# Optimization experiments

Hardware: AMD Instinct MI355X
Metric: run time of the kernel (lower is better)

The kernel has to match this reference:

```python
import jax, jax.numpy as jnp
import numpy as np

NUM_TAGS = 9
INNER_DIM = 64
HIDDEN = 768
MASK_VAL = 1e12


def setup_inputs() -> dict:
    key = jax.random.key(0)
    k1, k2, k3, k4 = jax.random.split(key, 4)
    B, S = 16, 512
    encoder_output = jax.random.normal(k1, (B, S, HIDDEN), dtype=jnp.float32)
    token_ids = jax.random.randint(k2, (B, S), 0, 30000, dtype=jnp.int64)
    attention_mask = jnp.ones((B, S), dtype=jnp.int32)
    W = jax.random.normal(k3, (HIDDEN, NUM_TAGS * INNER_DIM * 2), dtype=jnp.float32) * 0.02
    b = jax.random.normal(k4, (NUM_TAGS * INNER_DIM * 2,), dtype=jnp.float32) * 0.02
    return {"encoder_output": encoder_output, "token_ids": token_ids,
            "attention_mask": attention_mask, "W": W, "b": b}


def _rope_sin_cos(seq_len, dim, dtype):
    # sinusoidal position embedding, interleaved then repeat_interleave(2)
    pos = jnp.arange(seq_len, dtype=dtype)[:, None]              # [S,1]
    inv = jnp.power(10000.0, -2.0 * jnp.arange(dim // 2, dtype=dtype) / dim)
    ang = pos * inv                                              # [S,d/2]
    sin = jnp.repeat(jnp.sin(ang), 2, axis=-1)                   # [S,d]
    cos = jnp.repeat(jnp.cos(ang), 2, axis=-1)                   # [S,d]
    return sin, cos


def _rotate_half(x):
    # stack([-x[...,1::2], x[...,::2]], -1).reshape(x.shape)
    x2 = jnp.stack([-x[..., 1::2], x[..., ::2]], axis=-1)
    return x2.reshape(x.shape)


def reference(encoder_output, token_ids, attention_mask, W, b):
    B, S, _ = encoder_output.shape
    d = INNER_DIM
    out = encoder_output @ W + b                                 # [B,S,T*2d]
    out = out.reshape(B, S, NUM_TAGS, 2 * d)
    qw, kw = out[..., :d], out[..., d:]                          # [B,S,T,d]

    sin, cos = _rope_sin_cos(S, d, encoder_output.dtype)
    sin = sin[None, :, None, :]                                  # [1,S,1,d]
    cos = cos[None, :, None, :]
    qw = qw * cos + _rotate_half(qw) * sin
    kw = kw * cos + _rotate_half(kw) * sin

    logits = jnp.einsum('bshd,bthd->bhst', qw, kw)               # [B,T,S,S]

    pad = attention_mask.astype(logits.dtype)[:, None, None, :]  # key-side mask
    logits = logits * pad - (1.0 - pad) * MASK_VAL
    tril = jnp.tril(jnp.ones((S, S), dtype=logits.dtype), -1)
    logits = logits - tril * MASK_VAL
    return logits / jnp.sqrt(jnp.asarray(d, logits.dtype))
```

## Files before the change

kernel.cpp:

```cpp
#include <hip/hip_runtime.h>

#define MASK_VALF 1000000000000.0f

typedef __attribute__((ext_vector_type(8))) short s16x8;
typedef __attribute__((ext_vector_type(4))) float f32x4;

__device__ __forceinline__ unsigned f2bf_u(float f) {
    union { float f; unsigned u; } v; v.f = f;
    return (v.u + 0x7FFFu + ((v.u >> 16) & 1u)) >> 16;
}
__device__ __forceinline__ short f2bf(float f) { return (short)(f2bf_u(f) & 0xFFFFu); }

#define GLOAD16(gp, lp) __builtin_amdgcn_global_load_lds( \
    (const __attribute__((address_space(1))) void*)(gp),  \
    (__attribute__((address_space(3))) void*)(lp), 16, 0, 0)

__global__ __launch_bounds__(256) void prep_all(
    const float* __restrict__ enc, short* __restrict__ encb,
    const float* __restrict__ W, short* __restrict__ wtb,
    float* __restrict__ scf)
{
    const int blk = blockIdx.x;
    const int t = threadIdx.x;
    if (blk < 6144) {
        int i = blk * 256 + t;
        float4 v = ((const float4*)enc)[i];
        short4 o;
        o.x = f2bf(v.x); o.y = f2bf(v.y); o.z = f2bf(v.z); o.w = f2bf(v.w);
        ((short4*)encb)[i] = o;
    } else if (blk < 7008) {
        __shared__ float tile[32][33];
        int tb = blk - 6144;
        int tbx = tb % 36;
        int tby = tb / 36;
        int tx = t & 31, ty = t >> 5;
#pragma unroll
        for (int r = 0; r < 4; ++r) {
            int row = ty + r * 8;
            tile[row][tx] = W[(tby * 32 + row) * 1152 + tbx * 32 + tx];
        }
        __syncthreads();
#pragma unroll
        for (int r = 0; r < 4; ++r) {
            int row = ty + r * 8;
            wtb[(size_t)(tbx * 32 + row) * 768 + tby * 32 + tx] = f2bf(tile[tx][row]);
        }
    } else {
        int id = (blk - 7008) * 256 + t;
        int pos = id >> 5, j = id & 31;
        float inv = powf(10000.0f, -2.0f * (float)j / 64.0f);
        float ang = (float)pos * inv;
        float s, c;
        sincosf(ang, &s, &c);
        scf[id * 2]     = c;
        scf[id * 2 + 1] = s;
    }
}

__global__ __launch_bounds__(256) void gemm1_rope(
    const short* __restrict__ A,
    const short* __restrict__ Bt,
    const float* __restrict__ bias,
    const float* __restrict__ scf,
    short* __restrict__ qk)
{
    __shared__ __align__(16) short As[128 * 32];
    __shared__ __align__(16) short Bs[128 * 32];
    const int t = threadIdx.x;
    const int w = t >> 6, lane = t & 63;
    const int lr = lane & 15, quad = lane >> 4;
    const int wm = w >> 1, wn = w & 1;
    const int m0 = blockIdx.y * 128;
    const int n0 = blockIdx.x * 128;

    f32x4 acc[4][4] = {};

    const short* gA = A  + (size_t)(m0 + (t >> 2)) * 768 + (t & 3) * 8;
    const short* gB = Bt + (size_t)(n0 + (t >> 2)) * 768 + (t & 3) * 8;
    short* lA0 = &As[w * 512];
    short* lA1 = &As[2048 + w * 512];
    short* lB0 = &Bs[w * 512];
    short* lB1 = &Bs[2048 + w * 512];

    for (int kt = 0; kt < 24; ++kt) {
        __syncthreads();
        GLOAD16(gA,            lA0);
        GLOAD16(gA + 64 * 768, lA1);
        GLOAD16(gB,            lB0);
        GLOAD16(gB + 64 * 768, lB1);
        gA += 32; gB += 32;
        __syncthreads();

        s16x8 af[4], bw[4];
#pragma unroll
        for (int i = 0; i < 4; ++i)
            af[i] = *(const s16x8*)&Bs[(wm * 64 + i * 16 + lr) * 32 + quad * 8];
#pragma unroll
        for (int j = 0; j < 4; ++j)
            bw[j] = *(const s16x8*)&As[(wn * 64 + j * 16 + lr) * 32 + quad * 8];
#pragma unroll
        for (int i = 0; i < 4; ++i)
#pragma unroll
            for (int j = 0; j < 4; ++j)
                acc[i][j] = __builtin_amdgcn_mfma_f32_16x16x32_bf16(af[i], bw[j], acc[i][j], 0, 0, 0);
    }

#pragma unroll
    for (int i = 0; i < 4; ++i) {
        const int colg0 = n0 + wm * 64 + i * 16 + quad * 4;
        const float4 bv = *(const float4*)&bias[colg0];
        const int tag = colg0 >> 7;
        const int qkf = (colg0 >> 6) & 1;
        const int dd0 = colg0 & 63;
        const int jj0 = dd0 >> 1;
        short* qbase = qk + ((size_t)tag * 2 + qkf) * 512 * 64 + dd0;
#pragma unroll
        for (int j = 0; j < 4; ++j) {
            const int rowg = m0 + wn * 64 + j * 16 + lr;
            const int bidx = rowg >> 9;
            const int pos  = rowg & 511;
            const float4 cs = *(const float4*)&scf[pos * 64 + jj0 * 2];
            float x0 = acc[i][j][0] + bv.x;
            float x1 = acc[i][j][1] + bv.y;
            float x2 = acc[i][j][2] + bv.z;
            float x3 = acc[i][j][3] + bv.w;
            float o0 = x0 * cs.x - x1 * cs.y;
            float o1 = x1 * cs.x + x0 * cs.y;
            float o2 = x2 * cs.z - x3 * cs.w;
            float o3 = x3 * cs.z + x2 * cs.w;
            int2 st;
            st.x = (int)(f2bf_u(o0) & 0xFFFFu) | (int)(f2bf_u(o1) << 16);
            st.y = (int)(f2bf_u(o2) & 0xFFFFu) | (int)(f2bf_u(o3) << 16);
            *(int2*)&qbase[((size_t)bidx * 9 * 2 * 512 + pos) * 64] = st;
        }
    }
}

__global__ __launch_bounds__(256) void gemm2_mask(
    const short* __restrict__ qk,
    const int* __restrict__ amask,
    float* __restrict__ out)
{
    __shared__ __align__(16) short Qs[128 * 64];
    __shared__ __align__(16) short Ks[128 * 64];
    const int t = threadIdx.x;
    const int w = t >> 6, lane = t & 63;
    const int lr = lane & 15, quad = lane >> 4;
    const int wm = w >> 1, wn = w & 1;
    const int bh = blockIdx.z;
    const int bidx = bh / 9;
    const int s0 = blockIdx.y * 128;
    const int t0 = blockIdx.x * 128;

    const short* qbase = qk + (size_t)bh * 2 * 512 * 64;
    const short* kbase = qbase + 512 * 64;

    const int row = t >> 3, col8 = (t & 7) * 8;
#pragma unroll
    for (int p = 0; p < 4; ++p) {
        GLOAD16(qbase + (size_t)(s0 + p * 32 + row) * 64 + col8, &Qs[p * 2048 + w * 512]);
        GLOAD16(kbase + (size_t)(t0 + p * 32 + row) * 64 + col8, &Ks[p * 2048 + w * 512]);
    }
    __syncthreads();

    f32x4 acc[4][4] = {};
#pragma unroll
    for (int kk = 0; kk < 64; kk += 32) {
        s16x8 af[4], bw[4];
#pragma unroll
        for (int i = 0; i < 4; ++i)
            af[i] = *(const s16x8*)&Ks[(wm * 64 + i * 16 + lr) * 64 + kk + quad * 8];
#pragma unroll
        for (int j = 0; j < 4; ++j)
            bw[j] = *(const s16x8*)&Qs[(wn * 64 + j * 16 + lr) * 64 + kk + quad * 8];
#pragma unroll
        for (int i = 0; i < 4; ++i)
#pragma unroll
            for (int j = 0; j < 4; ++j)
                acc[i][j] = __builtin_amdgcn_mfma_f32_16x16x32_bf16(af[i], bw[j], acc[i][j], 0, 0, 0);
    }

#pragma unroll
    for (int i = 0; i < 4; ++i) {
        const int tg0 = t0 + wm * 64 + i * 16 + quad * 4;
        const int4 am = *(const int4*)&amask[bidx * 512 + tg0];
        const float4 pad = make_float4((float)am.x, (float)am.y, (float)am.z, (float)am.w);
        const float4 mk = make_float4((1.0f - pad.x) * MASK_VALF, (1.0f - pad.y) * MASK_VALF,
                                      (1.0f - pad.z) * MASK_VALF, (1.0f - pad.w) * MASK_VALF);
#pragma unroll
        for (int j = 0; j < 4; ++j) {
            const int sg = s0 + wn * 64 + j * 16 + lr;
            float4 v;
            v.x = (acc[i][j][0] * pad.x - mk.x - (sg > tg0     ? MASK_VALF : 0.0f)) * 0.125f;
            v.y = (acc[i][j][1] * pad.y - mk.y - (sg > tg0 + 1 ? MASK_VALF : 0.0f)) * 0.125f;
            v.z = (acc[i][j][2] * pad.z - mk.z - (sg > tg0 + 2 ? MASK_VALF : 0.0f)) * 0.125f;
            v.w = (acc[i][j][3] * pad.w - mk.w - (sg > tg0 + 3 ? MASK_VALF : 0.0f)) * 0.125f;
            *(float4*)&out[((size_t)bh * 512 + sg) * 512 + tg0] = v;
        }
    }
}

extern "C" void kernel_launch(void* const* d_in, const int* in_sizes, int n_in,
                              void* d_out, int out_size, void* d_ws, size_t ws_size,
                              hipStream_t stream) {
    const float* enc   = (const float*)d_in[0];
    const int*   amask = (const int*)d_in[2];
    const float* W     = (const float*)d_in[3];
    const float* bias  = (const float*)d_in[4];
    float* out = (float*)d_out;

    char* ws = (char*)d_ws;
    short* encb = (short*)(ws);
    short* wtb  = (short*)(ws + 12582912);
    float* scf  = (float*)(ws + 14352384);
    short* qk   = (short*)(ws + 14483456);

    prep_all  <<<7072, 256, 0, stream>>>(enc, encb, W, wtb, scf);
    gemm1_rope<<<dim3(9, 64), 256, 0, stream>>>(encb, wtb, bias, scf, qk);
    gemm2_mask<<<dim3(4, 4, 144), 256, 0, stream>>>(qk, amask, out);
}
```

Baseline: 225.9 us.

## Double-buffer GEMM1 LDS tiles and switch to 32x32x16 MFMA

The projection GEMM now double-buffers its LDS tiles so that the next K-slice's global-to-LDS loads are issued before the current slice is computed, and it drops one barrier per iteration. The MFMA shape moves from 16x16x32 to 32x32x16 with 2x2 fragments per wave, which reduces LDS fragment reads per MFMA. The epilogue is rewritten for the 32x32 accumulator layout. This doubles LDS usage and relies on the async global_load_lds having landed by the next barrier.

After: 229.1 us. About the same (+1.4%).

```diff
diff --git a/kernel.cpp b/kernel.cpp
--- a/kernel.cpp
+++ b/kernel.cpp
@@ -4,6 +4,7 @@
 
 typedef __attribute__((ext_vector_type(8))) short s16x8;
 typedef __attribute__((ext_vector_type(4))) float f32x4;
+typedef __attribute__((ext_vector_type(16))) float f32x16;
 
 __device__ __forceinline__ unsigned f2bf_u(float f) {
     union { float f; unsigned u; } v; v.f = f;
@@ -64,74 +65,87 @@
     const float* __restrict__ scf,
     short* __restrict__ qk)
 {
-    __shared__ __align__(16) short As[128 * 32];
-    __shared__ __align__(16) short Bs[128 * 32];
+    __shared__ __align__(16) short As[2][128 * 32];
+    __shared__ __align__(16) short Bs[2][128 * 32];
     const int t = threadIdx.x;
     const int w = t >> 6, lane = t & 63;
-    const int lr = lane & 15, quad = lane >> 4;
-    const int wm = w >> 1, wn = w & 1;
+    const int l31 = lane & 31, lh = lane >> 5;
+    const int wn2 = w & 1, wm2 = w >> 1;
     const int m0 = blockIdx.y * 128;
     const int n0 = blockIdx.x * 128;
 
-    f32x4 acc[4][4] = {};
+    f32x16 acc[2][2] = {};
 
     const short* gA = A  + (size_t)(m0 + (t >> 2)) * 768 + (t & 3) * 8;
     const short* gB = Bt + (size_t)(n0 + (t >> 2)) * 768 + (t & 3) * 8;
-    short* lA0 = &As[w * 512];
-    short* lA1 = &As[2048 + w * 512];
-    short* lB0 = &Bs[w * 512];
-    short* lB1 = &Bs[2048 + w * 512];
-
-    for (int kt = 0; kt < 24; ++kt) {
+
+    GLOAD16(gA,            &As[0][w * 512]);
+    GLOAD16(gA + 64 * 768, &As[0][2048 + w * 512]);
+    GLOAD16(gB,            &Bs[0][w * 512]);
+    GLOAD16(gB + 64 * 768, &Bs[0][2048 + w * 512]);
+    gA += 32; gB += 32;
+
+    auto compute = [&](const short* as, const short* bs) {
+        s16x8 af[2][2], bf[2][2];
+#pragma unroll
+        for (int fi = 0; fi < 2; ++fi)
+#pragma unroll
+            for (int kk = 0; kk < 2; ++kk) {
+                af[fi][kk] = *(const s16x8*)&bs[(wn2 * 64 + fi * 32 + l31) * 32 + kk * 16 + lh * 8];
+                bf[fi][kk] = *(const s16x8*)&as[(wm2 * 64 + fi * 32 + l31) * 32 + kk * 16 + lh * 8];
+            }
+#pragma unroll
+        for (int kk = 0; kk < 2; ++kk)
+#pragma unroll
+            for (int fi = 0; fi < 2; ++fi)
+#pragma unroll
+                for (int fj = 0; fj < 2; ++fj)
+                    acc[fi][fj] = __builtin_amdgcn_mfma_f32_32x32x16_bf16(
+                        af[fi][kk], bf[fj][kk], acc[fi][fj], 0, 0, 0);
+    };
+
+    for (int kt = 0; kt < 23; ++kt) {
         __syncthreads();
-        GLOAD16(gA,            lA0);
-        GLOAD16(gA + 64 * 768, lA1);
-        GLOAD16(gB,            lB0);
-        GLOAD16(gB + 64 * 768, lB1);
+        const int cur = kt & 1, nxt = cur ^ 1;
+        GLOAD16(gA,            &As[nxt][w * 512]);
+        GLOAD16(gA + 64 * 768, &As[nxt][2048 + w * 512]);
+        GLOAD16(gB,            &Bs[nxt][w * 512]);
+        GLOAD16(gB + 64 * 768, &Bs[nxt][2048 + w * 512]);
         gA += 32; gB += 32;
-        __syncthreads();
-
-        s16x8 af[4], bw[4];
-#pragma unroll
-        for (int i = 0; i < 4; ++i)
-            af[i] = *(const s16x8*)&Bs[(wm * 64 + i * 16 + lr) * 32 + quad * 8];
-#pragma unroll
-        for (int j = 0; j < 4; ++j)
-            bw[j] = *(const s16x8*)&As[(wn * 64 + j * 16 + lr) * 32 + quad * 8];
-#pragma unroll
-        for (int i = 0; i < 4; ++i)
-#pragma unroll
-            for (int j = 0; j < 4; ++j)
-                acc[i][j] = __builtin_amdgcn_mfma_f32_16x16x32_bf16(af[i], bw[j], acc[i][j], 0, 0, 0);
-    }
-
-#pragma unroll
-    for (int i = 0; i < 4; ++i) {
-        const int colg0 = n0 + wm * 64 + i * 16 + quad * 4;
-        const float4 bv = *(const float4*)&bias[colg0];
-        const int tag = colg0 >> 7;
-        const int qkf = (colg0 >> 6) & 1;
-        const int dd0 = colg0 & 63;
-        const int jj0 = dd0 >> 1;
-        short* qbase = qk + ((size_t)tag * 2 + qkf) * 512 * 64 + dd0;
-#pragma unroll
-        for (int j = 0; j < 4; ++j) {
-            const int rowg = m0 + wn * 64 + j * 16 + lr;
+        compute(As[cur], Bs[cur]);
+    }
+    __syncthreads();
+    compute(As[1], Bs[1]);
+
+#pragma unroll
+    for (int fi = 0; fi < 2; ++fi) {
+        const int n_base = n0 + wn2 * 64 + fi * 32;
+#pragma unroll
+        for (int fj = 0; fj < 2; ++fj) {
+            const int rowg = m0 + wm2 * 64 + fj * 32 + l31;
             const int bidx = rowg >> 9;
             const int pos  = rowg & 511;
-            const float4 cs = *(const float4*)&scf[pos * 64 + jj0 * 2];
-            float x0 = acc[i][j][0] + bv.x;
-            float x1 = acc[i][j][1] + bv.y;
-            float x2 = acc[i][j][2] + bv.z;
-            float x3 = acc[i][j][3] + bv.w;
-            float o0 = x0 * cs.x - x1 * cs.y;
-            float o1 = x1 * cs.x + x0 * cs.y;
-            float o2 = x2 * cs.z - x3 * cs.w;
-            float o3 = x3 * cs.z + x2 * cs.w;
-            int2 st;
-            st.x = (int)(f2bf_u(o0) & 0xFFFFu) | (int)(f2bf_u(o1) << 16);
-            st.y = (int)(f2bf_u(o2) & 0xFFFFu) | (int)(f2bf_u(o3) << 16);
-            *(int2*)&qbase[((size_t)bidx * 9 * 2 * 512 + pos) * 64] = st;
+#pragma unroll
+            for (int g = 0; g < 4; ++g) {
+                const int colg0 = n_base + g * 8 + lh * 4;
+                const float4 bv = *(const float4*)&bias[colg0];
+                const int tag = colg0 >> 7;
+                const int qkf = (colg0 >> 6) & 1;
+                const int dd0 = colg0 & 63;
+                const float4 cs = *(const float4*)&scf[pos * 64 + dd0];
+                float x0 = acc[fi][fj][g * 4 + 0] + bv.x;
+                float x1 = acc[fi][fj][g * 4 + 1] + bv.y;
+                float x2 = acc[fi][fj][g * 4 + 2] + bv.z;
+                float x3 = acc[fi][fj][g * 4 + 3] + bv.w;
+                float o0 = x0 * cs.x - x1 * cs.y;
+                float o1 = x1 * cs.x + x0 * cs.y;
+                float o2 = x2 * cs.z - x3 * cs.w;
+                float o3 = x3 * cs.z + x2 * cs.w;
+                int2 st;
+                st.x = (int)(f2bf_u(o0) & 0xFFFFu) | (int)(f2bf_u(o1) << 16);
+                st.y = (int)(f2bf_u(o2) & 0xFFFFu) | (int)(f2bf_u(o3) << 16);
+                *(int2*)&qk[((((size_t)bidx * 9 + tag) * 2 + qkf) * 512 + pos) * 64 + dd0] = st;
+            }
         }
     }
 }
```
